# Kernel optimization log

Hardware: AMD Instinct MI355X
Metric: run time of the kernel (lower is better)

Reference implementation:

```python
import jax, jax.numpy as jnp
import numpy as np

B, N, C = 2, 3072, 768
H = 12                      # num_heads
HD = C // H                 # 64
D = HD // 2                 # 32, rope dim per axis
GRID_H, GRID_W = 48, 64     # 768/16, 1024/16 ; GRID_H*GRID_W == N
BASE = 100.0
EPS = 1e-5


def _rope_tables():
    # positions per token (row-major cartesian product of y,x)
    pos_y = np.repeat(np.arange(GRID_H), GRID_W)   # [N]
    pos_x = np.tile(np.arange(GRID_W), GRID_H)     # [N]
    seq_len = max(GRID_H, GRID_W)
    inv_freq = 1.0 / BASE ** (np.arange(0, D, 2, dtype=np.float32) / D)  # [D/2]
    t = np.arange(seq_len, dtype=np.float32)
    freqs = np.einsum('i,j->ij', t, inv_freq)            # [S, D/2]
    emb = np.concatenate([freqs, freqs], axis=-1)        # [S, D]
    cos, sin = np.cos(emb), np.sin(emb)
    # gather per-token, add head broadcast dims -> [1, 1, N, D]
    mk = lambda tbl, idx: jnp.asarray(tbl[idx][None, None], dtype=jnp.float32)
    return mk(cos, pos_x), mk(sin, pos_x), mk(cos, pos_y), mk(sin, pos_y)


def setup_inputs() -> dict:
    key = jax.random.key(0)
    ks = jax.random.split(key, 12)
    s = 0.02
    cos_x, sin_x, cos_y, sin_y = _rope_tables()
    return {
        'x': jax.random.normal(ks[0], (B, N, C), jnp.float32),
        'w_qkv': jax.random.normal(ks[1], (3 * C, C), jnp.float32) * s,
        'w_proj': jax.random.normal(ks[2], (C, C), jnp.float32) * s,
        'b_proj': jnp.zeros((C,), jnp.float32),
        'g1': jnp.ones((C,), jnp.float32),
        'beta1': jnp.zeros((C,), jnp.float32),
        'g2': jnp.ones((C,), jnp.float32),
        'beta2': jnp.zeros((C,), jnp.float32),
        'w_fc1': jax.random.normal(ks[3], (4 * C, C), jnp.float32) * s,
        'b_fc1': jnp.zeros((4 * C,), jnp.float32),
        'w_fc2': jax.random.normal(ks[4], (C, 4 * C), jnp.float32) * s,
        'b_fc2': jnp.zeros((C,), jnp.float32),
        'cos_x': cos_x, 'sin_x': sin_x, 'cos_y': cos_y, 'sin_y': sin_y,
    }


def _layernorm(x, g, b):
    m = x.mean(-1, keepdims=True)
    v = ((x - m) ** 2).mean(-1, keepdims=True)
    return (x - m) * jax.lax.rsqrt(v + EPS) * g + b


def _rope1d(tok, cos, sin):
    t1, t2 = jnp.split(tok, 2, axis=-1)
    rot = jnp.concatenate([-t2, t1], axis=-1)
    return tok * cos + rot * sin


def _rope2d(tok, cos_x, sin_x, cos_y, sin_y):
    # tok: [B, H, N, HD]; first half of HD is y-coords, second half x-coords
    ty, tx = jnp.split(tok, 2, axis=-1)
    return jnp.concatenate([_rope1d(ty, cos_y, sin_y), _rope1d(tx, cos_x, sin_x)], axis=-1)


def reference(x, w_qkv, w_proj, b_proj, g1, beta1, g2, beta2,
              w_fc1, b_fc1, w_fc2, b_fc2, cos_x, sin_x, cos_y, sin_y):
    # --- attention branch ---
    xn = _layernorm(x, g1, beta1)
    qkv = jnp.einsum('bnc,dc->bnd', xn, w_qkv)           # [B, N, 3C]
    qkv = qkv.reshape(B, N, 3, H, HD).transpose(0, 3, 2, 1, 4)  # [B, H, 3, N, HD]
    q, k, v = qkv[:, :, 0], qkv[:, :, 1], qkv[:, :, 2]
    q = _rope2d(q, cos_x, sin_x, cos_y, sin_y)
    k = _rope2d(k, cos_x, sin_x, cos_y, sin_y)
    scale = HD ** -0.5
    attn = jnp.einsum('bhqd,bhkd->bhqk', q, k) * scale   # [B, H, N, N]
    attn = jax.nn.softmax(attn, axis=-1)
    o = jnp.einsum('bhqk,bhkd->bhqd', attn, v)           # [B, H, N, HD]
    o = o.transpose(0, 2, 1, 3).reshape(B, N, C)
    o = jnp.einsum('bnc,dc->bnd', o, w_proj) + b_proj
    x = x + o
    # --- mlp branch ---
    xn = _layernorm(x, g2, beta2)
    h = jnp.einsum('bnc,hc->bnh', xn, w_fc1) + b_fc1
    h = jax.nn.gelu(h, approximate=False)                # torch nn.GELU default (erf)
    h = jnp.einsum('bnh,ch->bnc', h, w_fc2) + b_fc2
    return x + h
```

## Files before the change

kernel.cpp:

```cpp
#include <hip/hip_runtime.h>
#include <hip/hip_bf16.h>


#define Nn 3072
#define Cc 768
#define Hh 12
#define Mm 6144

typedef unsigned short ushort_t;
typedef unsigned int u32;
using s8v = __attribute__((ext_vector_type(8))) short;
using f4v = __attribute__((ext_vector_type(4))) float;

__device__ __forceinline__ ushort_t f2b(float x){
  u32 u = __float_as_uint(x);
  return (ushort_t)((u + 0x7fffu + ((u >> 16) & 1u)) >> 16);
}
__device__ __forceinline__ u32 pack2(float a, float b){
  return (u32)f2b(a) | ((u32)f2b(b) << 16);
}
__device__ __forceinline__ u32 pack2t(float a, float b){
  return (__float_as_uint(a) >> 16) | (__float_as_uint(b) & 0xffff0000u);
}
__device__ __forceinline__ float b2f(ushort_t u){
  return __uint_as_float(((u32)u) << 16);
}

#define GLD16(g, l) __builtin_amdgcn_global_load_lds( \
    (const __attribute__((address_space(1))) u32*)(g), \
    (__attribute__((address_space(3))) u32*)(l), 16, 0, 0)

__global__ __launch_bounds__(256) void cvt4_kernel(
    const float* __restrict__ a, ushort_t* __restrict__ oa, int na,
    const float* __restrict__ b, ushort_t* __restrict__ ob, int nb,
    const float* __restrict__ c, ushort_t* __restrict__ oc, int nc,
    const float* __restrict__ d, ushort_t* __restrict__ od)
{
  int i = (blockIdx.x*256 + threadIdx.x)*4;
  const float* src; ushort_t* dst;
  if (i < na)           { src = a + i;            dst = oa + i; }
  else if (i < na+nb)   { src = b + (i-na);       dst = ob + (i-na); }
  else if (i < na+nb+nc){ src = c + (i-na-nb);    dst = oc + (i-na-nb); }
  else                  { src = d + (i-na-nb-nc); dst = od + (i-na-nb-nc); }
  float4 v = *(const float4*)src;
  uint2 p; p.x = pack2(v.x, v.y); p.y = pack2(v.z, v.w);
  *(uint2*)dst = p;
}

__global__ __launch_bounds__(256) void ln_kernel(const float* __restrict__ in,
    const float* __restrict__ g, const float* __restrict__ be, ushort_t* __restrict__ out)
{
  int row = blockIdx.x;
  int tid = threadIdx.x;
  size_t base = (size_t)row * Cc;
  float v[3];
  #pragma unroll
  for (int i = 0; i < 3; ++i) v[i] = in[base + tid + i*256];
  __shared__ float red[8];
  float s = v[0]+v[1]+v[2];
  #pragma unroll
  for (int off=32; off; off>>=1) s += __shfl_xor(s, off);
  int wid = tid >> 6, lane = tid & 63;
  if (lane==0) red[wid] = s;
  __syncthreads();
  float mean = (red[0]+red[1]+red[2]+red[3]) * (1.f/Cc);
  float d = 0.f;
  #pragma unroll
  for (int i=0;i<3;++i){ float t = v[i]-mean; d += t*t; }
  #pragma unroll
  for (int off=32; off; off>>=1) d += __shfl_xor(d, off);
  if (lane==0) red[4+wid] = d;
  __syncthreads();
  float var  = (red[4]+red[5]+red[6]+red[7]) * (1.f/Cc);
  float rstd = rsqrtf(var + 1e-5f);
  #pragma unroll
  for (int i=0;i<3;++i){
    int idx = tid + i*256;
    out[base+idx] = f2b((v[i]-mean)*rstd*g[idx] + be[idx]);
  }
}

template<int EPI, int NT>
__global__ __launch_bounds__(256) void mgemm_kernel(
    const ushort_t* __restrict__ A, const ushort_t* __restrict__ W,
    const float* __restrict__ bias, const float* __restrict__ residf,
    void* __restrict__ outv, int Nd, int K)
{
  constexpr int JT = NT/32;
  __shared__ __align__(16) ushort_t As[128*32];
  __shared__ __align__(16) ushort_t Ws[NT*32];
  int tid = threadIdx.x;
  int w = tid >> 6, lane = tid & 63;
  int g = lane >> 4, c = lane & 15;
  int wr = w >> 1, wc = w & 1;
  int gx = gridDim.x;
  int nwg = gx * gridDim.y;
  int lin = blockIdx.y * gx + blockIdx.x;
  int swz = (lin & 7) * (nwg >> 3) + (lin >> 3);
  int bx = swz % gx, by = swz / gx;
  int m0 = by * 128, n0 = bx * NT;
  int schunk = (lane & 3) * 8;
  const ushort_t* Ag = A + (size_t)(m0 + w*32 + (lane >> 2))*K + schunk;
  const ushort_t* Wg;
  if constexpr (NT == 128) Wg = W + (size_t)(n0 + w*32 + (lane >> 2))*K + schunk;
  else                     Wg = W + (size_t)(n0 + w*16 + (lane >> 2))*K + schunk;
  ushort_t* Asl = &As[w*1024];
  ushort_t* Wsl = (NT == 128) ? &Ws[w*1024] : &Ws[w*512];
  f4v acc[4][JT] = {};
  for (int k0 = 0; k0 < K; k0 += 32) {
    __syncthreads();
    GLD16(Ag + k0,        Asl);
    GLD16(Ag + 16*K + k0, Asl + 512);
    GLD16(Wg + k0,        Wsl);
    if constexpr (NT == 128) GLD16(Wg + 16*K + k0, Wsl + 512);
    __syncthreads();
    s8v af[4], wf[JT];
    #pragma unroll
    for (int i=0;i<4;++i) af[i] = *(const s8v*)&As[(wr*64 + i*16 + c)*32 + g*8];
    #pragma unroll
    for (int j=0;j<JT;++j) wf[j] = *(const s8v*)&Ws[(wc*(NT/2) + j*16 + c)*32 + g*8];
    #pragma unroll
    for (int i=0;i<4;++i)
      #pragma unroll
      for (int j=0;j<JT;++j)
        acc[i][j] = __builtin_amdgcn_mfma_f32_16x16x32_bf16(af[i], wf[j], acc[i][j], 0,0,0);
  }
  #pragma unroll
  for (int j=0;j<JT;++j){
    int col = n0 + wc*(NT/2) + j*16 + c;
    float bv = (EPI != 0) ? bias[col] : 0.f;
    #pragma unroll
    for (int i=0;i<4;++i){
      int row0 = m0 + wr*64 + i*16 + g*4;
      #pragma unroll
      for (int r=0;r<4;++r){
        float v = acc[i][j][r];
        size_t off = (size_t)(row0 + r)*Nd + col;
        if (EPI == 0) {
          ((ushort_t*)outv)[off] = f2b(v);
        } else if (EPI == 2) {
          float t = v + bv;
          ((ushort_t*)outv)[off] = f2b(0.5f*t*(1.0f + erff(t*0.70710678118654752f)));
        } else {
          ((float*)outv)[off] = v + bv + residf[off];
        }
      }
    }
  }
}

__global__ __launch_bounds__(256) void repack_kernel(
    const ushort_t* __restrict__ qkv,
    const float* __restrict__ cx, const float* __restrict__ sx,
    const float* __restrict__ cy, const float* __restrict__ sy,
    ushort_t* __restrict__ Qb, ushort_t* __restrict__ Kb, ushort_t* __restrict__ Vt)
{
  __shared__ float Vls[64*68];
  int bh = blockIdx.y;
  int b = bh / Hh, h = bh - b*Hh;
  int n0 = blockIdx.x * 64;
  int tid = threadIdx.x;
  int tt = tid >> 2, cch = tid & 3;
  int n = n0 + tt;
  size_t rowbase = (size_t)(b*Nn + n) * 2304 + h*64;

  int half = cch >> 1, ibase = (cch & 1) * 8;
  int d1 = half*32 + ibase;
  const float* ct  = half ? cx : cy;
  const float* st_ = half ? sx : sy;
  float c1[8], s1[8], c2[8], s2[8];
  #pragma unroll
  for (int j=0;j<8;++j){
    c1[j] = ct[n*32 + ibase + j];       s1[j] = st_[n*32 + ibase + j];
    c2[j] = ct[n*32 + ibase + 16 + j];  s2[j] = st_[n*32 + ibase + 16 + j];
  }
  #pragma unroll
  for (int qk = 0; qk < 2; ++qk){
    const ushort_t* src = qkv + rowbase + qk*768;
    uint4 uv1 = *(const uint4*)(src + d1);
    uint4 uv2 = *(const uint4*)(src + d1 + 16);
    float v1[8], v2[8];
    v1[0]=b2f(uv1.x&0xffff); v1[1]=b2f(uv1.x>>16); v1[2]=b2f(uv1.y&0xffff); v1[3]=b2f(uv1.y>>16);
    v1[4]=b2f(uv1.z&0xffff); v1[5]=b2f(uv1.z>>16); v1[6]=b2f(uv1.w&0xffff); v1[7]=b2f(uv1.w>>16);
    v2[0]=b2f(uv2.x&0xffff); v2[1]=b2f(uv2.x>>16); v2[2]=b2f(uv2.y&0xffff); v2[3]=b2f(uv2.y>>16);
    v2[4]=b2f(uv2.z&0xffff); v2[5]=b2f(uv2.z>>16); v2[6]=b2f(uv2.w&0xffff); v2[7]=b2f(uv2.w>>16);
    float sc = qk ? 1.0f : 0.18033688011112042f;
    float o1[8], o2[8];
    #pragma unroll
    for (int j=0;j<8;++j){
      o1[j] = (v1[j]*c1[j] - v2[j]*s1[j]) * sc;
      o2[j] = (v2[j]*c2[j] + v1[j]*s2[j]) * sc;
    }
    ushort_t* dst = (qk ? Kb : Qb) + ((size_t)bh*Nn + n)*64;
    uint4 u1, u2;
    u1.x = pack2(o1[0],o1[1]); u1.y = pack2(o1[2],o1[3]);
    u1.z = pack2(o1[4],o1[5]); u1.w = pack2(o1[6],o1[7]);
    u2.x = pack2(o2[0],o2[1]); u2.y = pack2(o2[2],o2[3]);
    u2.z = pack2(o2[4],o2[5]); u2.w = pack2(o2[6],o2[7]);
    *(uint4*)(dst + d1)      = u1;
    *(uint4*)(dst + d1 + 16) = u2;
  }

  {
    const ushort_t* src = qkv + rowbase + 1536 + cch*16;
    uint4 ua = *(const uint4*)(src);
    uint4 ub = *(const uint4*)(src + 8);
    float* lp = &Vls[tt*68 + cch*16];
    lp[0]=b2f(ua.x&0xffff); lp[1]=b2f(ua.x>>16); lp[2]=b2f(ua.y&0xffff); lp[3]=b2f(ua.y>>16);
    lp[4]=b2f(ua.z&0xffff); lp[5]=b2f(ua.z>>16); lp[6]=b2f(ua.w&0xffff); lp[7]=b2f(ua.w>>16);
    lp[8]=b2f(ub.x&0xffff); lp[9]=b2f(ub.x>>16); lp[10]=b2f(ub.y&0xffff); lp[11]=b2f(ub.y>>16);
    lp[12]=b2f(ub.z&0xffff); lp[13]=b2f(ub.z>>16); lp[14]=b2f(ub.w&0xffff); lp[15]=b2f(ub.w>>16);
  }
  __syncthreads();
  {
    int d = tid & 63, quarter = tid >> 6;
    float v[16];
    #pragma unroll
    for (int j=0;j<16;++j) v[j] = Vls[(quarter*16 + j)*68 + d];
    uint4 w0, w1;
    w0.x = pack2(v[0],v[1]);   w0.y = pack2(v[2],v[3]);
    w0.z = pack2(v[4],v[5]);   w0.w = pack2(v[6],v[7]);
    w1.x = pack2(v[8],v[9]);   w1.y = pack2(v[10],v[11]);
    w1.z = pack2(v[12],v[13]); w1.w = pack2(v[14],v[15]);
    ushort_t* dst = Vt + ((size_t)bh*64 + d)*Nn + n0 + quarter*16;
    *(uint4*)(dst)     = w0;
    *(uint4*)(dst + 8) = w1;
  }
}

__global__ __launch_bounds__(256, 3) void fattn_kernel(
    const ushort_t* __restrict__ Qb, const ushort_t* __restrict__ Kb,
    const ushort_t* __restrict__ Vt, ushort_t* __restrict__ ob)
{
  __shared__ __align__(16) char smem[36864];
  __shared__ float Lred[256];
  int bh = blockIdx.x;
  int q0 = blockIdx.y * 64;
  int tid = threadIdx.x;
  int w = tid >> 6, lane = tid & 63, g = lane >> 4, c = lane & 15;

  const ushort_t* kbase = Kb + (size_t)bh*Nn*64;
  const ushort_t* vbase = Vt + (size_t)bh*64*Nn;

  s8v qf0[4], qf1[4];
  #pragma unroll
  for (int qs=0;qs<4;++qs){
    const ushort_t* qp = Qb + ((size_t)bh*Nn + q0 + qs*16 + c)*64;
    qf0[qs] = *(const s8v*)(qp + g*8);
    qf1[qs] = *(const s8v*)(qp + 32 + g*8);
  }
  s8v ones8;
  #pragma unroll
  for (int j=0;j<8;++j) ones8[j] = (short)0x3f80;

  f4v o[4][4] = {};
  f4v l[4] = {};
  ushort_t* pw = (ushort_t*)smem + w*4608;

  for (int it = 0; it < 12; ++it){
    int key0 = (it*4 + w) * 64;
    s8v ka[4], kb2[4];
    #pragma unroll
    for (int ks=0;ks<4;++ks){
      const ushort_t* kr = kbase + (size_t)(key0 + ks*16 + c)*64 + g*8;
      ka[ks]  = *(const s8v*)(kr);
      kb2[ks] = *(const s8v*)(kr + 32);
    }
    #pragma unroll
    for (int qs=0;qs<4;++qs){
      #pragma unroll
      for (int ks=0;ks<4;++ks){
        f4v z = {0,0,0,0};
        z = __builtin_amdgcn_mfma_f32_16x16x32_bf16(ka[ks],  qf0[qs], z, 0,0,0);
        z = __builtin_amdgcn_mfma_f32_16x16x32_bf16(kb2[ks], qf1[qs], z, 0,0,0);
        uint2 pk;
        pk.x = pack2t(__builtin_amdgcn_exp2f(z[0]), __builtin_amdgcn_exp2f(z[1]));
        pk.y = pack2t(__builtin_amdgcn_exp2f(z[2]), __builtin_amdgcn_exp2f(z[3]));
        *(uint2*)&pw[qs*1152 + c*72 + ks*16 + g*4] = pk;
      }
    }
    asm volatile("s_waitcnt lgkmcnt(0)" ::: "memory");
    s8v va[4], vb[4];
    #pragma unroll
    for (int d=0;d<4;++d){
      const ushort_t* vr = vbase + (size_t)(d*16 + c)*Nn + key0 + g*8;
      va[d] = *(const s8v*)(vr);
      vb[d] = *(const s8v*)(vr + 32);
    }
    #pragma unroll
    for (int qs=0;qs<4;++qs){
      s8v pf0 = *(const s8v*)&pw[qs*1152 + c*72 + g*8];
      s8v pf1 = *(const s8v*)&pw[qs*1152 + c*72 + 32 + g*8];
      #pragma unroll
      for (int d=0;d<4;++d){
        o[qs][d] = __builtin_amdgcn_mfma_f32_16x16x32_bf16(va[d], pf0, o[qs][d], 0,0,0);
        o[qs][d] = __builtin_amdgcn_mfma_f32_16x16x32_bf16(vb[d], pf1, o[qs][d], 0,0,0);
      }
      l[qs] = __builtin_amdgcn_mfma_f32_16x16x32_bf16(ones8, pf0, l[qs], 0,0,0);
      l[qs] = __builtin_amdgcn_mfma_f32_16x16x32_bf16(ones8, pf1, l[qs], 0,0,0);
    }
  }

  ushort_t* Or = (ushort_t*)smem;
  #pragma unroll
  for (int qs=0;qs<4;++qs){
    #pragma unroll
    for (int d=0;d<4;++d){
      uint2 pk;
      pk.x = pack2(o[qs][d][0], o[qs][d][1]);
      pk.y = pack2(o[qs][d][2], o[qs][d][3]);
      *(uint2*)&Or[(w*64 + qs*16 + c)*72 + d*16 + g*4] = pk;
    }
    Lred[w*64 + qs*16 + c] = l[qs][0];
  }
  __syncthreads();

  int qrow = tid >> 2, dseg = (tid & 3) * 16;
  float acc[16] = {};
  #pragma unroll
  for (int w2=0;w2<4;++w2){
    const ushort_t* base = &Or[(w2*64 + qrow)*72 + dseg];
    uint4 u0 = *(const uint4*)(base);
    uint4 u1 = *(const uint4*)(base + 8);
    u32 uu[8] = {u0.x,u0.y,u0.z,u0.w,u1.x,u1.y,u1.z,u1.w};
    #pragma unroll
    for (int j=0;j<8;++j){
      acc[j*2]   += b2f((ushort_t)(uu[j] & 0xffff));
      acc[j*2+1] += b2f((ushort_t)(uu[j] >> 16));
    }
  }
  float rl = 1.0f / (Lred[qrow] + Lred[64+qrow] + Lred[128+qrow] + Lred[192+qrow]);
  int b = bh / Hh, h = bh - b*Hh;
  ushort_t* op = ob + ((size_t)b*Nn + q0 + qrow)*768 + h*64 + dseg;
  uint4 w0_, w1_;
  w0_.x = pack2(acc[0]*rl, acc[1]*rl);   w0_.y = pack2(acc[2]*rl, acc[3]*rl);
  w0_.z = pack2(acc[4]*rl, acc[5]*rl);   w0_.w = pack2(acc[6]*rl, acc[7]*rl);
  w1_.x = pack2(acc[8]*rl, acc[9]*rl);   w1_.y = pack2(acc[10]*rl, acc[11]*rl);
  w1_.z = pack2(acc[12]*rl, acc[13]*rl); w1_.w = pack2(acc[14]*rl, acc[15]*rl);
  *(uint4*)(op)     = w0_;
  *(uint4*)(op + 8) = w1_;
}

extern "C" void kernel_launch(void* const* d_in, const int* in_sizes, int n_in,
                              void* d_out, int out_size, void* d_ws, size_t ws_size,
                              hipStream_t stream)
{
  const float* x      = (const float*)d_in[0];
  const float* w_qkv  = (const float*)d_in[1];
  const float* w_proj = (const float*)d_in[2];
  const float* b_proj = (const float*)d_in[3];
  const float* g1     = (const float*)d_in[4];
  const float* be1    = (const float*)d_in[5];
  const float* g2     = (const float*)d_in[6];
  const float* be2    = (const float*)d_in[7];
  const float* w_fc1  = (const float*)d_in[8];
  const float* b_fc1  = (const float*)d_in[9];
  const float* w_fc2  = (const float*)d_in[10];
  const float* b_fc2  = (const float*)d_in[11];
  const float* cx     = (const float*)d_in[12];
  const float* sx     = (const float*)d_in[13];
  const float* cy     = (const float*)d_in[14];
  const float* sy     = (const float*)d_in[15];
  float* out = (float*)d_out;

  char* ws = (char*)d_ws;
  ushort_t* xnb   = (ushort_t*)(ws);
  ushort_t* Qb    = (ushort_t*)(ws + 9437184);
  ushort_t* Kb    = (ushort_t*)(ws + 18874368);
  float*    x1    = (float*)   (ws + 9437184);
  ushort_t* Vt    = (ushort_t*)(ws + 28311552);
  ushort_t* obb   = (ushort_t*)(ws + 37748736);
  ushort_t* qkvb  = (ushort_t*)(ws + 47185920);
  ushort_t* hb    = (ushort_t*)(ws + 47185920);
  ushort_t* wqkvb = (ushort_t*)(ws + 84934656);
  ushort_t* wprojb= (ushort_t*)(ws + 88473600);
  ushort_t* wfc1b = (ushort_t*)(ws + 89653248);
  ushort_t* wfc2b = (ushort_t*)(ws + 94371840);

  cvt4_kernel<<<(7077888/4)/256, 256, 0, stream>>>(
      w_qkv, wqkvb, 2304*768, w_proj, wprojb, 768*768,
      w_fc1, wfc1b, 3072*768, w_fc2, wfc2b);

  ln_kernel<<<Mm, 256, 0, stream>>>(x, g1, be1, xnb);
  mgemm_kernel<0,128><<<dim3(2304/128, Mm/128), 256, 0, stream>>>(xnb, wqkvb, nullptr, nullptr, qkvb, 2304, 768);
  repack_kernel<<<dim3(48, 24), 256, 0, stream>>>(qkvb, cx, sx, cy, sy, Qb, Kb, Vt);
  fattn_kernel<<<dim3(24, 48), 256, 0, stream>>>(Qb, Kb, Vt, obb);
  mgemm_kernel<1,64><<<dim3(768/64, Mm/128), 256, 0, stream>>>(obb, wprojb, b_proj, x, x1, 768, 768);
  ln_kernel<<<Mm, 256, 0, stream>>>(x1, g2, be2, xnb);
  mgemm_kernel<2,128><<<dim3(3072/128, Mm/128), 256, 0, stream>>>(xnb, wfc1b, b_fc1, nullptr, hb, 3072, 768);
  mgemm_kernel<1,64><<<dim3(768/64, Mm/128), 256, 0, stream>>>(hb, wfc2b, b_fc2, x1, out, 768, 3072);
}
```

Measured before the change: 448.9 us.

## Double-buffer LDS tiles in the GEMM kernel to overlap global loads with MFMA

Gives the A and W tiles of the bf16 GEMM two LDS buffers each. The loads for the next K-step are issued before the MFMAs on the current buffer, and each iteration now ends with a single barrier instead of two. The aim is to hide global-to-LDS latency behind compute. In exchange, the kernel uses twice the LDS, which may lower occupancy. It also relies on GLD16 (presumably an async global-to-LDS load) having completed by the time the barrier is reached.

Result: faster. 438.4 us (-2.3%).

```diff
diff --git a/kernel.cpp b/kernel.cpp
--- a/kernel.cpp
+++ b/kernel.cpp
@@ -87,8 +87,8 @@
     void* __restrict__ outv, int Nd, int K)
 {
   constexpr int JT = NT/32;
-  __shared__ __align__(16) ushort_t As[128*32];
-  __shared__ __align__(16) ushort_t Ws[NT*32];
+  __shared__ __align__(16) ushort_t As[2][128*32];
+  __shared__ __align__(16) ushort_t Ws[2][NT*32];
   int tid = threadIdx.x;
   int w = tid >> 6, lane = tid & 63;
   int g = lane >> 4, c = lane & 15;
@@ -104,26 +104,39 @@
   const ushort_t* Wg;
   if constexpr (NT == 128) Wg = W + (size_t)(n0 + w*32 + (lane >> 2))*K + schunk;
   else                     Wg = W + (size_t)(n0 + w*16 + (lane >> 2))*K + schunk;
-  ushort_t* Asl = &As[w*1024];
-  ushort_t* Wsl = (NT == 128) ? &Ws[w*1024] : &Ws[w*512];
+  int wAoff = w*1024;
+  int wWoff = (NT == 128) ? w*1024 : w*512;
   f4v acc[4][JT] = {};
-  for (int k0 = 0; k0 < K; k0 += 32) {
-    __syncthreads();
-    GLD16(Ag + k0,        Asl);
-    GLD16(Ag + 16*K + k0, Asl + 512);
-    GLD16(Wg + k0,        Wsl);
-    if constexpr (NT == 128) GLD16(Wg + 16*K + k0, Wsl + 512);
-    __syncthreads();
+
+  {
+    GLD16(Ag,        &As[0][wAoff]);
+    GLD16(Ag + 16*K, &As[0][wAoff + 512]);
+    GLD16(Wg,        &Ws[0][wWoff]);
+    if constexpr (NT == 128) GLD16(Wg + 16*K, &Ws[0][wWoff + 512]);
+  }
+  __syncthreads();
+
+  int nk = K >> 5;
+  for (int t = 0; t < nk; ++t) {
+    int cur = t & 1;
+    if (t + 1 < nk) {
+      int k1 = (t + 1) << 5;
+      GLD16(Ag + k1,        &As[cur^1][wAoff]);
+      GLD16(Ag + 16*K + k1, &As[cur^1][wAoff + 512]);
+      GLD16(Wg + k1,        &Ws[cur^1][wWoff]);
+      if constexpr (NT == 128) GLD16(Wg + 16*K + k1, &Ws[cur^1][wWoff + 512]);
+    }
     s8v af[4], wf[JT];
     #pragma unroll
-    for (int i=0;i<4;++i) af[i] = *(const s8v*)&As[(wr*64 + i*16 + c)*32 + g*8];
-    #pragma unroll
-    for (int j=0;j<JT;++j) wf[j] = *(const s8v*)&Ws[(wc*(NT/2) + j*16 + c)*32 + g*8];
+    for (int i=0;i<4;++i) af[i] = *(const s8v*)&As[cur][(wr*64 + i*16 + c)*32 + g*8];
+    #pragma unroll
+    for (int j=0;j<JT;++j) wf[j] = *(const s8v*)&Ws[cur][(wc*(NT/2) + j*16 + c)*32 + g*8];
     #pragma unroll
     for (int i=0;i<4;++i)
       #pragma unroll
       for (int j=0;j<JT;++j)
         acc[i][j] = __builtin_amdgcn_mfma_f32_16x16x32_bf16(af[i], wf[j], acc[i][j], 0,0,0);
+    __syncthreads();
   }
   #pragma unroll
   for (int j=0;j<JT;++j){
```
